# Kernel optimization log

Hardware: AMD Instinct MI355X
Metric: run time of the kernel (lower is better)

## Reference

```python
import jax, jax.numpy as jnp
import numpy as np

B, S, D, H = 2, 2048, 2048, 16
HD = D // H  # head_dim = 128

def _rope_tables(head_dim, context_length, theta_base=10000.0):
    inv_freq = 1.0 / theta_base ** (jnp.arange(0, head_dim, 2, dtype=jnp.float32) / head_dim)
    pos = jnp.arange(context_length, dtype=jnp.float32)
    angles = pos[:, None] * inv_freq[None, :]            # [S, HD/2]
    angles = jnp.concatenate([angles, angles], axis=1)   # [S, HD]
    return jnp.cos(angles), jnp.sin(angles)

def _apply_rope(x, cos, sin):
    # x: [b, h, s, hd]; cos/sin: [s, hd]
    hd = x.shape[-1]
    x1, x2 = x[..., : hd // 2], x[..., hd // 2 :]
    rotated = jnp.concatenate([-x2, x1], axis=-1)
    return x * cos[None, None] + rotated * sin[None, None]

def setup_inputs() -> dict:
    key = jax.random.key(0)
    ks = jax.random.split(key, 5)
    x = jax.random.normal(ks[0], (B, S, D), dtype=jnp.float32)
    scale = 1.0 / np.sqrt(D)
    Wq = jax.random.normal(ks[1], (D, D), dtype=jnp.float32) * scale
    Wk = jax.random.normal(ks[2], (D, D), dtype=jnp.float32) * scale
    Wv = jax.random.normal(ks[3], (D, D), dtype=jnp.float32) * scale
    Wo = jax.random.normal(ks[4], (D, D), dtype=jnp.float32) * scale
    cos, sin = _rope_tables(HD, S)
    return {"x": x, "Wq": Wq, "Wk": Wk, "Wv": Wv, "Wo": Wo, "cos": cos, "sin": sin}

def reference(x, Wq, Wk, Wv, Wo, cos, sin):
    b, s, _ = x.shape
    def split_heads(t):  # [b,s,D] -> [b,H,s,HD]
        return t.reshape(b, s, H, HD).transpose(0, 2, 1, 3)
    q = split_heads(x @ Wq.T)
    k = split_heads(x @ Wk.T)
    v = split_heads(x @ Wv.T)
    q = _apply_rope(q, cos[:s], sin[:s])
    k = _apply_rope(k, cos[:s], sin[:s])
    scores = jnp.einsum("bhqd,bhkd->bhqk", q, k) / np.sqrt(HD)
    causal = jnp.triu(jnp.ones((s, s), dtype=bool), k=1)
    scores = jnp.where(causal[None, None], -jnp.inf, scores)
    weights = jax.nn.softmax(scores, axis=-1)
    ctx = jnp.einsum("bhqk,bhkd->bhqd", weights, v)
    ctx = ctx.transpose(0, 2, 1, 3).reshape(b, s, D)
    return ctx @ Wo.T
```

## Files before the change

kernel.cpp:

```cpp
#include <hip/hip_runtime.h>
#include <cstdint>
#include <cmath>

#define B_ 2
#define S_ 2048
#define D_ 2048
#define H_ 16
#define HD_ 128

#define NEG_SENTINEL -1.0e30f

typedef __bf16 bf16;
typedef __attribute__((ext_vector_type(4))) __bf16 bf16x4;
typedef __attribute__((ext_vector_type(8))) __bf16 bf16x8;
typedef __attribute__((ext_vector_type(4))) float f32x4;

__device__ __forceinline__ void gload_lds16(const void* g, void* l) {
  __builtin_amdgcn_global_load_lds(
      (const __attribute__((address_space(1))) unsigned int*)g,
      (__attribute__((address_space(3))) unsigned int*)l, 16, 0, 0);
}

__device__ __forceinline__ f32x4 mfma16(bf16x8 a, bf16x8 b, f32x4 c) {
  return __builtin_amdgcn_mfma_f32_16x16x32_bf16(a, b, c, 0, 0, 0);
}

__global__ __launch_bounds__(256) void cvt_f32_bf16(
    const float* __restrict__ in, bf16* __restrict__ out)
{
  int i = blockIdx.x * 256 + threadIdx.x;
  f32x4 v = ((const f32x4*)in)[i];
  bf16x4 o;
#pragma unroll
  for (int j = 0; j < 4; ++j) o[j] = (bf16)v[j];
  ((bf16x4*)out)[i] = o;
}

#define GTM 128
#define GTN 128
#define GBK 64

template <typename OT>
__global__ __launch_bounds__(256) void gemm_xwt(
    const bf16* __restrict__ A, const bf16* __restrict__ W, OT* __restrict__ C,
    int M, int N, int K, int ldc)
{
  __shared__ bf16 sA[GTM * GBK];
  __shared__ bf16 sB[GTN * GBK];
  const int tid  = threadIdx.x;
  const int wave = tid >> 6, lane = tid & 63;
  const int quad = lane >> 4, l16 = lane & 15;
  const int tm = blockIdx.y * GTM;
  const int tn = blockIdx.x * GTN;
  const int wm = (wave >> 1) * 64, wn = (wave & 1) * 64;

  f32x4 acc[4][4];
#pragma unroll
  for (int i = 0; i < 4; ++i)
#pragma unroll
    for (int j = 0; j < 4; ++j) acc[i][j] = (f32x4)0.0f;

  for (int k0 = 0; k0 < K; k0 += GBK) {
    __syncthreads();
#pragma unroll
    for (int g = 0; g < 4; ++g) {
      int gb  = (g * 4 + wave) * 64;
      int p   = gb + lane;
      int row = p >> 3, pos = p & 7;
      int cc  = pos ^ (row & 7);
      gload_lds16(A + (size_t)(tm + row) * K + k0 + cc * 8, (char*)sA + (size_t)gb * 16);
      gload_lds16(W + (size_t)(tn + row) * K + k0 + cc * 8, (char*)sB + (size_t)gb * 16);
    }
    __syncthreads();

#pragma unroll
    for (int t = 0; t < 2; ++t) {
      bf16x8 af[4], bfr[4];
#pragma unroll
      for (int i = 0; i < 4; ++i) {
        int rowa = wm + i * 16 + l16;
        int posa = (t * 4 + quad) ^ (rowa & 7);
        af[i] = *(const bf16x8*)(sA + rowa * GBK + posa * 8);
        int rowb = wn + i * 16 + l16;
        int posb = (t * 4 + quad) ^ (rowb & 7);
        bfr[i] = *(const bf16x8*)(sB + rowb * GBK + posb * 8);
      }
#pragma unroll
      for (int i = 0; i < 4; ++i)
#pragma unroll
        for (int j = 0; j < 4; ++j)
          acc[i][j] = mfma16(af[i], bfr[j], acc[i][j]);
    }
  }

#pragma unroll
  for (int i = 0; i < 4; ++i)
#pragma unroll
    for (int r = 0; r < 4; ++r) {
      int row = tm + wm + i * 16 + quad * 4 + r;
#pragma unroll
      for (int j = 0; j < 4; ++j) {
        int col = tn + wn + j * 16 + l16;
        C[(size_t)row * ldc + col] = (OT)acc[i][j][r];
      }
    }
}

__global__ __launch_bounds__(256) void rope_qk(
    bf16* __restrict__ Q, bf16* __restrict__ Kk,
    const float* __restrict__ cosT, const float* __restrict__ sinT, int rs)
{
  const float kappa = 0.08838834764831845f * 1.4426950408889634f;
  int t = blockIdx.x * 256 + threadIdx.x;
  int d = t & 63;
  int h = (t >> 6) & (H_ - 1);
  int s = (t >> 10) & (S_ - 1);
  int b = t >> 21;
  size_t base = ((size_t)(b * S_ + s)) * rs + (size_t)h * HD_;
  float c1 = cosT[s * HD_ + d];
  float s1 = sinT[s * HD_ + d];
  float c2 = cosT[s * HD_ + d + 64];
  float s2 = sinT[s * HD_ + d + 64];
  {
    float x1 = (float)Q[base + d], x2 = (float)Q[base + d + 64];
    Q[base + d]      = (bf16)((x1 * c1 - x2 * s1) * kappa);
    Q[base + d + 64] = (bf16)((x2 * c2 + x1 * s2) * kappa);
  }
  {
    float x1 = (float)Kk[base + d], x2 = (float)Kk[base + d + 64];
    Kk[base + d]      = (bf16)(x1 * c1 - x2 * s1);
    Kk[base + d + 64] = (bf16)(x2 * c2 + x1 * s2);
  }
}

__global__ __launch_bounds__(256) void transpose_v(
    const bf16* __restrict__ V, bf16* __restrict__ Vt, int rs)
{
  __shared__ bf16 sT[64 * 72];
  const int tid = threadIdx.x;
  const int si = blockIdx.x;
  const int di = blockIdx.y;
  const int bh = blockIdx.z;
  const int b  = bh >> 4, h = bh & 15;

  const bf16* src = V + (size_t)b * S_ * rs + (size_t)h * HD_ + di * 64;
  bf16*       dst = Vt + ((size_t)bh * HD_ + di * 64) * S_ + si * 64;

#pragma unroll
  for (int half = 0; half < 2; ++half) {
    int r  = half * 32 + (tid >> 3);
    int c0 = (tid & 7) * 8;
    bf16x8 v = *(const bf16x8*)(src + (size_t)(si * 64 + r) * rs + c0);
    *(bf16x8*)(sT + r * 72 + c0) = v;
  }
  __syncthreads();
#pragma unroll
  for (int half = 0; half < 2; ++half) {
    int dr = half * 32 + (tid >> 3);
    int c0 = (tid & 7) * 8;
    bf16x8 o;
#pragma unroll
    for (int j = 0; j < 8; ++j) o[j] = sT[(c0 + j) * 72 + dr];
    *(bf16x8*)(dst + (size_t)dr * S_ + c0) = o;
  }
}

#define ABK 64
#define SPS 72

__global__ __launch_bounds__(256) void attn_fwd(
    const bf16* __restrict__ Q, const bf16* __restrict__ K,
    const bf16* __restrict__ Vt, bf16* __restrict__ O, int rs)
{
  __shared__ bf16 sK[ABK * HD_];
  __shared__ bf16 sVT[HD_ * ABK];
  __shared__ bf16 sP[64 * SPS];

  const int tid  = threadIdx.x;
  const int wave = tid >> 6, lane = tid & 63;
  const int quad = lane >> 4, l16 = lane & 15;

  const int lin   = (int)blockIdx.x;
  const int low3  = lin & 7;
  const int rest  = lin >> 3;
  const int pairx = rest & 15;
  const int colhi = rest >> 4;
  const int col   = low3 + (colhi << 3);
  const int b = col >> 4, h = col & 15;

  const bf16* Qh  = Q + (size_t)b * S_ * rs + (size_t)h * HD_;
  const bf16* Kh  = K + (size_t)b * S_ * rs + (size_t)h * HD_;
  const bf16* Vth = Vt + ((size_t)(b * H_ + h) * HD_) * S_;
  bf16*       Oh  = O + (size_t)b * S_ * D_ + (size_t)h * HD_;

  const int wq = wave * 16;

#pragma unroll 1
  for (int seg = 0; seg < 2; ++seg) {
    const int qt = seg == 0 ? pairx : 31 - pairx;
    const int q0 = qt * 64;
    const int wq_abs = q0 + wq;

    bf16x8 qf[4];
    {
      const bf16* rp = Qh + (size_t)(wq_abs + l16) * rs + quad * 8;
#pragma unroll
      for (int t = 0; t < 4; ++t) qf[t] = *(const bf16x8*)(rp + t * 32);
    }

    f32x4 o_acc[8];
#pragma unroll
    for (int j = 0; j < 8; ++j) o_acc[j] = (f32x4)0.0f;
    float m_col = NEG_SENTINEL;
    float l_col = 0.0f;

    const int nkt = qt + 1;
#pragma unroll 1
    for (int kt = 0; kt < nkt; ++kt) {
      const int kk0 = kt * ABK;
      __syncthreads();

#pragma unroll
      for (int g = 0; g < 4; ++g) {
        int p   = g * 256 + tid;
        int row = p >> 4, pos = p & 15;
        int cc  = pos ^ (row & 15);
        gload_lds16(Kh + (size_t)(kk0 + row) * rs + cc * 8, (char*)sK + (size_t)p * 16);
      }
#pragma unroll
      for (int g = 0; g < 4; ++g) {
        int p  = g * 256 + tid;
        int d  = p >> 3, pos = p & 7;
        int cc = pos ^ (d & 7);
        gload_lds16(Vth + (size_t)d * S_ + kk0 + cc * 8, (char*)sVT + (size_t)p * 16);
      }
      __syncthreads();

      if (kk0 <= wq_abs + 15) {
        f32x4 st[4];
#pragma unroll
        for (int jt = 0; jt < 4; ++jt) {
          bf16x8 kf[4];
#pragma unroll
          for (int t = 0; t < 4; ++t) {
            int pos = (t * 4 + quad) ^ l16;
            kf[t] = *(const bf16x8*)(sK + (jt * 16 + l16) * HD_ + pos * 8);
          }
          f32x4 a = (f32x4)0.0f;
#pragma unroll
          for (int t = 0; t < 4; ++t) a = mfma16(kf[t], qf[t], a);
          st[jt] = a;
        }

        if (kk0 + 63 > wq_abs) {
          int qcol = wq_abs + l16;
#pragma unroll
          for (int jt = 0; jt < 4; ++jt)
#pragma unroll
            for (int r = 0; r < 4; ++r) {
              int key = kk0 + jt * 16 + quad * 4 + r;
              if (key > qcol) st[jt][r] = NEG_SENTINEL;
            }
        }

        float mx = NEG_SENTINEL;
#pragma unroll
        for (int jt = 0; jt < 4; ++jt)
#pragma unroll
          for (int r = 0; r < 4; ++r) mx = fmaxf(mx, st[jt][r]);
        mx = fmaxf(mx, __shfl_xor(mx, 16, 64));
        mx = fmaxf(mx, __shfl_xor(mx, 32, 64));
        float m_new = fmaxf(m_col, mx);
        float alpha = exp2f(m_col - m_new);
        float ts = 0.0f;
#pragma unroll
        for (int jt = 0; jt < 4; ++jt) {
          bf16x4 pk;
#pragma unroll
          for (int r = 0; r < 4; ++r) {
            float p = exp2f(st[jt][r] - m_new);
            ts += p;
            pk[r] = (bf16)p;
          }
          *(bf16x4*)(sP + (wq + l16) * SPS + jt * 16 + quad * 4) = pk;
        }
        ts += __shfl_xor(ts, 16, 64);
        ts += __shfl_xor(ts, 32, 64);
        l_col = l_col * alpha + ts;
        m_col = m_new;
#pragma unroll
        for (int r = 0; r < 4; ++r) {
          float av = __shfl(alpha, quad * 4 + r, 64);
#pragma unroll
          for (int jd = 0; jd < 8; ++jd) o_acc[jd][r] *= av;
        }

#pragma unroll
        for (int ks = 0; ks < 2; ++ks) {
          bf16x8 pf = *(const bf16x8*)(sP + (wq + l16) * SPS + ks * 32 + quad * 8);
#pragma unroll
          for (int jd = 0; jd < 8; ++jd) {
            int pos = (ks * 4 + quad) ^ (l16 & 7);
            bf16x8 vf = *(const bf16x8*)(sVT + (jd * 16 + l16) * ABK + pos * 8);
            o_acc[jd] = mfma16(pf, vf, o_acc[jd]);
          }
        }
      }
    }

#pragma unroll
    for (int r = 0; r < 4; ++r) {
      float lv = __shfl(l_col, quad * 4 + r, 64);
      float inv_l = 1.0f / lv;
      int row = wq_abs + quad * 4 + r;
#pragma unroll
      for (int jd = 0; jd < 8; ++jd) {
        int colo = jd * 16 + l16;
        Oh[(size_t)row * D_ + colo] = (bf16)(o_acc[jd][r] * inv_l);
      }
    }
  }
}

extern "C" void kernel_launch(void* const* d_in, const int* in_sizes, int n_in,
                              void* d_out, int out_size, void* d_ws, size_t ws_size,
                              hipStream_t stream) {
  const float* x    = (const float*)d_in[0];
  const float* Wq   = (const float*)d_in[1];
  const float* Wk   = (const float*)d_in[2];
  const float* Wv   = (const float*)d_in[3];
  const float* Wo   = (const float*)d_in[4];
  const float* cosT = (const float*)d_in[5];
  const float* sinT = (const float*)d_in[6];
  float* out = (float*)d_out;

  const size_t NE = (size_t)B_ * S_ * D_;
  const size_t WE = (size_t)D_ * D_;
  const int M = B_ * S_;
  const int cvtX = (int)(NE / 1024);
  const int cvtW = (int)(WE / 1024);

  if (ws_size >= (size_t)92274688) {
    bf16* QKV   = (bf16*)d_ws;
    bf16* xb    = QKV + (size_t)M * 6144;
    bf16* Wqkv  = xb + NE;
    bf16* ctx   = Wqkv;
    bf16* Wob   = Wqkv + 2 * WE;
    bf16* Vt    = xb;

    cvt_f32_bf16<<<cvtX, 256, 0, stream>>>(x, xb);
    cvt_f32_bf16<<<cvtW, 256, 0, stream>>>(Wq, Wqkv);
    cvt_f32_bf16<<<cvtW, 256, 0, stream>>>(Wk, Wqkv + WE);
    cvt_f32_bf16<<<cvtW, 256, 0, stream>>>(Wv, Wqkv + 2 * WE);
    gemm_xwt<bf16><<<dim3(48, 32), 256, 0, stream>>>(xb, Wqkv, QKV, M, 3 * D_, D_, 3 * D_);
    rope_qk<<<(B_ * S_ * H_ * 64) / 256, 256, 0, stream>>>(QKV, QKV + D_, cosT, sinT, 3 * D_);
    transpose_v<<<dim3(32, 2, 32), 256, 0, stream>>>(QKV + 2 * D_, Vt, 3 * D_);
    attn_fwd<<<512, 256, 0, stream>>>(QKV, QKV + D_, Vt, ctx, 3 * D_);
    cvt_f32_bf16<<<cvtW, 256, 0, stream>>>(Wo, Wob);
    gemm_xwt<float><<<dim3(16, 32), 256, 0, stream>>>(ctx, Wob, out, M, D_, D_, D_);
  } else {
    bf16* Qb    = (bf16*)d_ws;
    bf16* Kb    = Qb + NE;
    bf16* Vb    = Kb + NE;
    bf16* Cb    = Vb + NE;
    bf16* Wslot = Cb + NE;

    cvt_f32_bf16<<<cvtX, 256, 0, stream>>>(x, Cb);
    cvt_f32_bf16<<<cvtW, 256, 0, stream>>>(Wq, Wslot);
    gemm_xwt<bf16><<<dim3(16, 32), 256, 0, stream>>>(Cb, Wslot, Qb, M, D_, D_, D_);
    cvt_f32_bf16<<<cvtW, 256, 0, stream>>>(Wk, Wslot);
    gemm_xwt<bf16><<<dim3(16, 32), 256, 0, stream>>>(Cb, Wslot, Kb, M, D_, D_, D_);
    cvt_f32_bf16<<<cvtW, 256, 0, stream>>>(Wv, Wslot);
    gemm_xwt<bf16><<<dim3(16, 32), 256, 0, stream>>>(Cb, Wslot, Vb, M, D_, D_, D_);
    rope_qk<<<(B_ * S_ * H_ * 64) / 256, 256, 0, stream>>>(Qb, Kb, cosT, sinT, D_);
    transpose_v<<<dim3(32, 2, 32), 256, 0, stream>>>(Vb, Cb, D_);
    attn_fwd<<<512, 256, 0, stream>>>(Qb, Kb, Cb, Vb, D_);
    cvt_f32_bf16<<<cvtW, 256, 0, stream>>>(Wo, Wslot);
    gemm_xwt<float><<<dim3(16, 32), 256, 0, stream>>>(Vb, Wslot, out, M, D_, D_, D_);
  }
}
```

Before: 402.8 us.

## Replace projection GEMMs with double-buffered 256x128 pipelined GEMM kernel

Adds a new gemm_pipe kernel with 512 threads, 256x128 tiles, double-buffered LDS staging through direct global-to-LDS loads, split half-tile prefetch, and s_setprio around the MFMA bursts. It uses an XCD-aware block remap to improve L2 locality. The fused QKV projection and the output projection switch to it on the large-workspace path. The aim is to overlap global loads with MFMA work and raise arithmetic intensity, at the cost of 96KB of dynamic LDS, which limits occupancy and makes the hand-tuned vmcnt waits fragile.

```diff
diff --git a/kernel.cpp b/kernel.cpp
--- a/kernel.cpp
+++ b/kernel.cpp
@@ -23,6 +23,12 @@
 
 __device__ __forceinline__ f32x4 mfma16(bf16x8 a, bf16x8 b, f32x4 c) {
   return __builtin_amdgcn_mfma_f32_16x16x32_bf16(a, b, c, 0, 0, 0);
+}
+
+__device__ __forceinline__ void wg_barrier() {
+  asm volatile("" ::: "memory");
+  __builtin_amdgcn_s_barrier();
+  asm volatile("" ::: "memory");
 }
 
 __global__ __launch_bounds__(256) void cvt_f32_bf16(
@@ -100,6 +106,138 @@
       int row = tm + wm + i * 16 + quad * 4 + r;
 #pragma unroll
       for (int j = 0; j < 4; ++j) {
+        int col = tn + wn + j * 16 + l16;
+        C[(size_t)row * ldc + col] = (OT)acc[i][j][r];
+      }
+    }
+}
+
+#define PTM 256
+#define PTN 128
+#define PBK 64
+#define PBUFB 49152
+#define PLDSB 98304
+
+#define STAGE_AU(kt_, u_) do { \
+    char* dstA_ = smem + (((kt_) & 1) * PBUFB); \
+    _Pragma("unroll") \
+    for (int g2_ = 0; g2_ < 2; ++g2_) { \
+      int row0_ = (u_) * 64 + g2_ * 128 + wave * 8; \
+      int row_  = row0_ + (lane >> 3); \
+      int cc_   = (lane & 7) ^ (row_ & 7); \
+      gload_lds16(A + (size_t)(tm + row_) * K + (size_t)(kt_) * PBK + cc_ * 8, \
+                  dstA_ + row0_ * 128); \
+    } } while (0)
+
+#define STAGE_BF(kt_) do { \
+    char* dstB_ = smem + (((kt_) & 1) * PBUFB) + 32768; \
+    _Pragma("unroll") \
+    for (int g2_ = 0; g2_ < 2; ++g2_) { \
+      int row0_ = g2_ * 64 + wave * 8; \
+      int row_  = row0_ + (lane >> 3); \
+      int cc_   = (lane & 7) ^ (row_ & 7); \
+      gload_lds16(W + (size_t)(tn + row_) * K + (size_t)(kt_) * PBK + cc_ * 8, \
+                  dstB_ + row0_ * 128); \
+    } } while (0)
+
+template <typename OT>
+__global__ __launch_bounds__(512, 2) void gemm_pipe(
+    const bf16* __restrict__ A, const bf16* __restrict__ W, OT* __restrict__ C,
+    int M, int N, int K, int ldc, int nby)
+{
+  extern __shared__ char smem[];
+  const int tid  = threadIdx.x;
+  const int wave = tid >> 6, lane = tid & 63;
+  const int quad = lane >> 4, l16 = lane & 15;
+
+  const int nwg = (int)gridDim.x;
+  const int cpx = nwg >> 3;
+  const int wg  = ((int)blockIdx.x & 7) * cpx + ((int)blockIdx.x >> 3);
+  const int bx = wg / nby, by = wg % nby;
+  const int tm = by * PTM, tn = bx * PTN;
+  const int wm = (wave >> 2) * 128, wn = (wave & 3) * 32;
+
+  const int NT = K / PBK;
+
+  f32x4 acc[8][2];
+#pragma unroll
+  for (int i = 0; i < 8; ++i)
+#pragma unroll
+    for (int j = 0; j < 2; ++j) acc[i][j] = (f32x4)0.0f;
+
+  STAGE_AU(0, 0);
+  STAGE_AU(0, 1);
+  STAGE_BF(0);
+  if (NT > 1) STAGE_AU(1, 0);
+  asm volatile("s_waitcnt vmcnt(2)" ::: "memory");
+  wg_barrier();
+
+#pragma unroll 1
+  for (int t = 0; t < NT; ++t) {
+    const bf16* sAb = (const bf16*)(smem + (t & 1) * PBUFB);
+    const bf16* sBb = sAb + 16384;
+    bf16x8 a[4][2], b[2][2];
+
+#pragma unroll
+    for (int i = 0; i < 4; ++i)
+#pragma unroll
+      for (int t2 = 0; t2 < 2; ++t2) {
+        int r  = wm + i * 16 + l16;
+        int ps = (t2 * 4 + quad) ^ (r & 7);
+        a[i][t2] = *(const bf16x8*)(sAb + r * 64 + ps * 8);
+      }
+#pragma unroll
+    for (int j = 0; j < 2; ++j)
+#pragma unroll
+      for (int t2 = 0; t2 < 2; ++t2) {
+        int r  = wn + j * 16 + l16;
+        int ps = (t2 * 4 + quad) ^ (r & 7);
+        b[j][t2] = *(const bf16x8*)(sBb + r * 64 + ps * 8);
+      }
+    if (t + 1 < NT) { STAGE_AU(t + 1, 1); STAGE_BF(t + 1); }
+    wg_barrier();
+    __builtin_amdgcn_s_setprio(1);
+#pragma unroll
+    for (int i = 0; i < 4; ++i)
+#pragma unroll
+      for (int j = 0; j < 2; ++j)
+#pragma unroll
+        for (int t2 = 0; t2 < 2; ++t2)
+          acc[i][j] = mfma16(a[i][t2], b[j][t2], acc[i][j]);
+    __builtin_amdgcn_s_setprio(0);
+    wg_barrier();
+
+#pragma unroll
+    for (int i = 0; i < 4; ++i)
+#pragma unroll
+      for (int t2 = 0; t2 < 2; ++t2) {
+        int r  = wm + 64 + i * 16 + l16;
+        int ps = (t2 * 4 + quad) ^ (r & 7);
+        a[i][t2] = *(const bf16x8*)(sAb + r * 64 + ps * 8);
+      }
+    if (t + 2 < NT) STAGE_AU(t + 2, 0);
+    wg_barrier();
+    __builtin_amdgcn_s_setprio(1);
+#pragma unroll
+    for (int i = 0; i < 4; ++i)
+#pragma unroll
+      for (int j = 0; j < 2; ++j)
+#pragma unroll
+        for (int t2 = 0; t2 < 2; ++t2)
+          acc[4 + i][j] = mfma16(a[i][t2], b[j][t2], acc[4 + i][j]);
+    __builtin_amdgcn_s_setprio(0);
+    if (t + 2 >= NT) { asm volatile("s_waitcnt vmcnt(0)" ::: "memory"); }
+    else             { asm volatile("s_waitcnt vmcnt(2)" ::: "memory"); }
+    wg_barrier();
+  }
+
+#pragma unroll
+  for (int i = 0; i < 8; ++i)
+#pragma unroll
+    for (int r = 0; r < 4; ++r) {
+      int row = tm + wm + i * 16 + quad * 4 + r;
+#pragma unroll
+      for (int j = 0; j < 2; ++j) {
         int col = tn + wn + j * 16 + l16;
         C[(size_t)row * ldc + col] = (OT)acc[i][j][r];
       }
@@ -340,6 +478,15 @@
   const int cvtX = (int)(NE / 1024);
   const int cvtW = (int)(WE / 1024);
 
+  static bool attr_done = false;
+  if (!attr_done) {
+    (void)hipFuncSetAttribute(reinterpret_cast<const void*>(gemm_pipe<bf16>),
+                              hipFuncAttributeMaxDynamicSharedMemorySize, PLDSB);
+    (void)hipFuncSetAttribute(reinterpret_cast<const void*>(gemm_pipe<float>),
+                              hipFuncAttributeMaxDynamicSharedMemorySize, PLDSB);
+    attr_done = true;
+  }
+
   if (ws_size >= (size_t)92274688) {
     bf16* QKV   = (bf16*)d_ws;
     bf16* xb    = QKV + (size_t)M * 6144;
@@ -352,12 +499,12 @@
     cvt_f32_bf16<<<cvtW, 256, 0, stream>>>(Wq, Wqkv);
     cvt_f32_bf16<<<cvtW, 256, 0, stream>>>(Wk, Wqkv + WE);
     cvt_f32_bf16<<<cvtW, 256, 0, stream>>>(Wv, Wqkv + 2 * WE);
-    gemm_xwt<bf16><<<dim3(48, 32), 256, 0, stream>>>(xb, Wqkv, QKV, M, 3 * D_, D_, 3 * D_);
+    gemm_pipe<bf16><<<768, 512, PLDSB, stream>>>(xb, Wqkv, QKV, M, 3 * D_, D_, 3 * D_, 16);
     rope_qk<<<(B_ * S_ * H_ * 64) / 256, 256, 0, stream>>>(QKV, QKV + D_, cosT, sinT, 3 * D_);
     transpose_v<<<dim3(32, 2, 32), 256, 0, stream>>>(QKV + 2 * D_, Vt, 3 * D_);
     attn_fwd<<<512, 256, 0, stream>>>(QKV, QKV + D_, Vt, ctx, 3 * D_);
     cvt_f32_bf16<<<cvtW, 256, 0, stream>>>(Wo, Wob);
-    gemm_xwt<float><<<dim3(16, 32), 256, 0, stream>>>(ctx, Wob, out, M, D_, D_, D_);
+    gemm_pipe<float><<<256, 512, PLDSB, stream>>>(ctx, Wob, out, M, D_, D_, D_, 16);
   } else {
     bf16* Qb    = (bf16*)d_ws;
     bf16* Kb    = Qb + NE;
```

Result: no change. 410.3 us (+1.9%).

## Replace QKV projection GEMM with 256x256 eight-phase pipelined kernel

Applied to the files above, without the earlier changes.

Adds a new bf16 GEMM for the fused QKV projection. It uses 256x256 tiles with 512 threads, double-buffered LDS loaded directly from global memory, and an eight-phase schedule that interleaves staging, LDS reads and MFMA under explicit waitcnt and barrier control. It also remaps workgroup IDs so blocks are grouped across dies. The aim is to hide global load latency and raise MFMA utilisation compared with the 128x128 GEMM. In exchange it needs 128KB of dynamic LDS and fragile hand-tuned wait counts, and the output projection still uses the old GEMM.

```diff
diff --git a/kernel.cpp b/kernel.cpp
--- a/kernel.cpp
+++ b/kernel.cpp
@@ -23,6 +23,12 @@
 
 __device__ __forceinline__ f32x4 mfma16(bf16x8 a, bf16x8 b, f32x4 c) {
   return __builtin_amdgcn_mfma_f32_16x16x32_bf16(a, b, c, 0, 0, 0);
+}
+
+__device__ __forceinline__ void wg_barrier() {
+  asm volatile("" ::: "memory");
+  __builtin_amdgcn_s_barrier();
+  asm volatile("" ::: "memory");
 }
 
 __global__ __launch_bounds__(256) void cvt_f32_bf16(
@@ -102,6 +108,192 @@
       for (int j = 0; j < 4; ++j) {
         int col = tn + wn + j * 16 + l16;
         C[(size_t)row * ldc + col] = (OT)acc[i][j][r];
+      }
+    }
+}
+
+#define QTM 256
+#define QTN 256
+#define QBK 64
+#define QHALF 16384
+#define QBUF 65536
+#define QLDS 131072
+
+#define QSTAGE_A(kt_, h_, bi_) do { \
+    char* dst_ = smem + (bi_) * QBUF + (h_) * QHALF; \
+    _Pragma("unroll") \
+    for (int g_ = 0; g_ < 2; ++g_) { \
+      int p_   = g_ * 512 + tid; \
+      int row_ = p_ >> 3; \
+      int cc_  = (p_ & 7) ^ (row_ & 7); \
+      gload_lds16(A + (size_t)(tm + (h_) * 128 + row_) * K + (size_t)(kt_) * QBK + cc_ * 8, \
+                  dst_ + (size_t)p_ * 16); \
+    } } while (0)
+
+#define QSTAGE_B(kt_, h_, bi_) do { \
+    char* dst_ = smem + (bi_) * QBUF + 32768 + (h_) * QHALF; \
+    _Pragma("unroll") \
+    for (int g_ = 0; g_ < 2; ++g_) { \
+      int p_   = g_ * 512 + tid; \
+      int row_ = p_ >> 3; \
+      int cc_  = (p_ & 7) ^ (row_ & 7); \
+      gload_lds16(W + (size_t)(tn + (h_) * 128 + row_) * K + (size_t)(kt_) * QBK + cc_ * 8, \
+                  dst_ + (size_t)p_ * 16); \
+    } } while (0)
+
+#define QREAD_A(Ab_, rh_) \
+    _Pragma("unroll") \
+    for (int i_ = 0; i_ < 4; ++i_) \
+    _Pragma("unroll") \
+    for (int t2_ = 0; t2_ < 2; ++t2_) { \
+      int rr_ = (rh_) * 64 + i_ * 16 + l16; \
+      int ps_ = (t2_ * 4 + quad) ^ (rr_ & 7); \
+      a[i_][t2_] = *(const bf16x8*)((Ab_) + rr_ * 64 + ps_ * 8); \
+    }
+
+#define QREAD_B(Bb_, bv_, ch_) \
+    _Pragma("unroll") \
+    for (int j_ = 0; j_ < 2; ++j_) \
+    _Pragma("unroll") \
+    for (int t2_ = 0; t2_ < 2; ++t2_) { \
+      int rb_ = wn64 + (ch_) * 32 + j_ * 16 + l16; \
+      int ps_ = (t2_ * 4 + quad) ^ (rb_ & 7); \
+      bv_[j_][t2_] = *(const bf16x8*)((Bb_) + rb_ * 64 + ps_ * 8); \
+    }
+
+#define QMFMA(rh_, ch_, bv_) \
+    __builtin_amdgcn_s_setprio(1); \
+    _Pragma("unroll") \
+    for (int i_ = 0; i_ < 4; ++i_) \
+    _Pragma("unroll") \
+    for (int j_ = 0; j_ < 2; ++j_) \
+    _Pragma("unroll") \
+    for (int t2_ = 0; t2_ < 2; ++t2_) \
+      acc[(rh_) * 4 + i_][(ch_) * 2 + j_] = \
+          mfma16(a[i_][t2_], bv_[j_][t2_], acc[(rh_) * 4 + i_][(ch_) * 2 + j_]); \
+    __builtin_amdgcn_s_setprio(0);
+
+#define LGK0()  asm volatile("s_waitcnt lgkmcnt(0)" ::: "memory")
+#define LGK8()  asm volatile("s_waitcnt lgkmcnt(8)" ::: "memory")
+#define VM4()   asm volatile("s_waitcnt vmcnt(4)" ::: "memory")
+#define VM0()   asm volatile("s_waitcnt vmcnt(0)" ::: "memory")
+
+__global__ __launch_bounds__(512, 2) void gemm_8ph(
+    const bf16* __restrict__ A, const bf16* __restrict__ W, bf16* __restrict__ C,
+    int M, int N, int K, int ldc, int nby)
+{
+  extern __shared__ char smem[];
+  const int tid  = threadIdx.x;
+  const int wave = tid >> 6, lane = tid & 63;
+  const int quad = lane >> 4, l16 = lane & 15;
+
+  const int nwg = (int)gridDim.x;
+  const int cpx = nwg >> 3;
+  const int wg  = ((int)blockIdx.x & 7) * cpx + ((int)blockIdx.x >> 3);
+  const int bx = wg / nby, by = wg % nby;
+  const int tm = by * QTM, tn = bx * QTN;
+  const int wm = (wave >> 2) * 128;
+  const int wn = (wave & 3) * 64;
+  const int wn64 = wn & 64;
+
+  const bf16* A0 = (const bf16*)(smem + (wm >> 7) * QHALF);
+  const bf16* B0 = (const bf16*)(smem + 32768 + (wn >> 7) * QHALF);
+  const bf16* A1 = (const bf16*)(smem + QBUF + (wm >> 7) * QHALF);
+  const bf16* B1 = (const bf16*)(smem + QBUF + 32768 + (wn >> 7) * QHALF);
+
+  const int NT = K / QBK;
+  const int NI = NT >> 1;
+
+  f32x4 acc[8][4];
+#pragma unroll
+  for (int i = 0; i < 8; ++i)
+#pragma unroll
+    for (int j = 0; j < 4; ++j) acc[i][j] = (f32x4)0.0f;
+
+  bf16x8 a[4][2], b0[2][2], b1[2][2];
+
+  QSTAGE_A(0, 0, 0);
+  QSTAGE_A(0, 1, 0);
+  QSTAGE_B(0, 0, 0);
+  QSTAGE_B(0, 1, 0);
+  QSTAGE_B(1, 0, 1);
+  QSTAGE_B(1, 1, 1);
+  VM4();
+  wg_barrier();
+
+#pragma unroll 1
+  for (int it = 0; it < NI; ++it) {
+    const int t0 = it * 2, t1 = t0 + 1;
+    const bool last = (it == NI - 1);
+
+    QREAD_A(A0, 0);
+    QREAD_B(B0, b0, 0);
+    QSTAGE_A(t1, 0, 1);
+    LGK8();
+    wg_barrier();
+    LGK0();
+    QMFMA(0, 0, b0);
+    wg_barrier();
+
+    QREAD_B(B0, b1, 1);
+    QSTAGE_A(t1, 1, 1);
+    wg_barrier();
+    LGK0();
+    QMFMA(0, 1, b1);
+    wg_barrier();
+
+    QREAD_A(A0, 1);
+    if (!last) QSTAGE_B(t0 + 2, 0, 0);
+    wg_barrier();
+    LGK0();
+    QMFMA(1, 1, b1);
+    wg_barrier();
+
+    if (!last) QSTAGE_B(t0 + 2, 1, 0);
+    wg_barrier();
+    QMFMA(1, 0, b0);
+    if (last) { VM0(); } else { VM4(); }
+    wg_barrier();
+
+    QREAD_A(A1, 0);
+    QREAD_B(B1, b0, 0);
+    if (!last) QSTAGE_A(t0 + 2, 0, 0);
+    LGK8();
+    wg_barrier();
+    LGK0();
+    QMFMA(0, 0, b0);
+    wg_barrier();
+
+    QREAD_B(B1, b1, 1);
+    if (!last) QSTAGE_A(t0 + 2, 1, 0);
+    wg_barrier();
+    LGK0();
+    QMFMA(0, 1, b1);
+    wg_barrier();
+
+    QREAD_A(A1, 1);
+    if (!last) QSTAGE_B(t1 + 2, 0, 1);
+    wg_barrier();
+    LGK0();
+    QMFMA(1, 1, b1);
+    wg_barrier();
+
+    if (!last) QSTAGE_B(t1 + 2, 1, 1);
+    wg_barrier();
+    QMFMA(1, 0, b0);
+    if (!last) { VM4(); }
+    wg_barrier();
+  }
+
+#pragma unroll
+  for (int ii = 0; ii < 8; ++ii)
+#pragma unroll
+    for (int r = 0; r < 4; ++r) {
+      int row = tm + wm + (ii >> 2) * 64 + (ii & 3) * 16 + quad * 4 + r;
+#pragma unroll
+      for (int jj = 0; jj < 4; ++jj) {
+        int col = tn + wn + jj * 16 + l16;
+        C[(size_t)row * ldc + col] = (bf16)acc[ii][jj][r];
       }
     }
 }
@@ -246,10 +438,10 @@
             int pos = (t * 4 + quad) ^ l16;
             kf[t] = *(const bf16x8*)(sK + (jt * 16 + l16) * HD_ + pos * 8);
           }
-          f32x4 a = (f32x4)0.0f;
-#pragma unroll
-          for (int t = 0; t < 4; ++t) a = mfma16(kf[t], qf[t], a);
-          st[jt] = a;
+          f32x4 a2 = (f32x4)0.0f;
+#pragma unroll
+          for (int t = 0; t < 4; ++t) a2 = mfma16(kf[t], qf[t], a2);
+          st[jt] = a2;
         }
 
         if (kk0 + 63 > wq_abs) {
@@ -340,6 +532,13 @@
   const int cvtX = (int)(NE / 1024);
   const int cvtW = (int)(WE / 1024);
 
+  static bool attr_done = false;
+  if (!attr_done) {
+    (void)hipFuncSetAttribute(reinterpret_cast<const void*>(gemm_8ph),
+                              hipFuncAttributeMaxDynamicSharedMemorySize, QLDS);
+    attr_done = true;
+  }
+
   if (ws_size >= (size_t)92274688) {
     bf16* QKV   = (bf16*)d_ws;
     bf16* xb    = QKV + (size_t)M * 6144;
@@ -352,7 +551,7 @@
     cvt_f32_bf16<<<cvtW, 256, 0, stream>>>(Wq, Wqkv);
     cvt_f32_bf16<<<cvtW, 256, 0, stream>>>(Wk, Wqkv + WE);
     cvt_f32_bf16<<<cvtW, 256, 0, stream>>>(Wv, Wqkv + 2 * WE);
-    gemm_xwt<bf16><<<dim3(48, 32), 256, 0, stream>>>(xb, Wqkv, QKV, M, 3 * D_, D_, 3 * D_);
+    gemm_8ph<<<384, 512, QLDS, stream>>>(xb, Wqkv, QKV, M, 3 * D_, D_, 3 * D_, 16);
     rope_qk<<<(B_ * S_ * H_ * 64) / 256, 256, 0, stream>>>(QKV, QKV + D_, cosT, sinT, 3 * D_);
     transpose_v<<<dim3(32, 2, 32), 256, 0, stream>>>(QKV + 2 * D_, Vt, 3 * D_);
     attn_fwd<<<512, 256, 0, stream>>>(QKV, QKV + D_, Vt, ctx, 3 * D_);
```

Measured after the change: 399.6 us. No clear change (-0.8%).

## Double-buffer K/V tiles in attention kernel with async prefetch

Applied to the files above, without the earlier changes.

Moves attention K and V^T staging into dynamic shared memory with two buffers. The next tile's global-to-LDS loads are issued before computing on the current tile, so load latency overlaps with the MFMA work. One waitcnt and barrier per iteration replace the two syncthreads around each load. The cost is roughly 73KB of LDS per block, which may lower occupancy to one or two blocks per CU.

```diff
diff --git a/kernel.cpp b/kernel.cpp
--- a/kernel.cpp
+++ b/kernel.cpp
@@ -24,6 +24,14 @@
 __device__ __forceinline__ f32x4 mfma16(bf16x8 a, bf16x8 b, f32x4 c) {
   return __builtin_amdgcn_mfma_f32_16x16x32_bf16(a, b, c, 0, 0, 0);
 }
+
+__device__ __forceinline__ void wg_barrier() {
+  asm volatile("" ::: "memory");
+  __builtin_amdgcn_s_barrier();
+  asm volatile("" ::: "memory");
+}
+
+#define AVM0() asm volatile("s_waitcnt vmcnt(0)" ::: "memory")
 
 __global__ __launch_bounds__(256) void cvt_f32_bf16(
     const float* __restrict__ in, bf16* __restrict__ out)
@@ -167,14 +175,36 @@
 
 #define ABK 64
 #define SPS 72
+#define ALDS 74752
+
+#define AK_STAGE(kt_, b_) do { \
+    int kk_ = (kt_) * ABK; \
+    _Pragma("unroll") \
+    for (int g_ = 0; g_ < 4; ++g_) { \
+      int p_   = g_ * 256 + tid; \
+      int row_ = p_ >> 4, pos_ = p_ & 15; \
+      int cc_  = pos_ ^ (row_ & 15); \
+      gload_lds16(Kh + (size_t)(kk_ + row_) * rs + cc_ * 8, \
+                  smem + (b_) * 16384 + (size_t)p_ * 16); \
+    } } while (0)
+
+#define AV_STAGE(kt_, b_) do { \
+    int kk_ = (kt_) * ABK; \
+    _Pragma("unroll") \
+    for (int g_ = 0; g_ < 4; ++g_) { \
+      int p_  = g_ * 256 + tid; \
+      int d_  = p_ >> 3, pos_ = p_ & 7; \
+      int cc_ = pos_ ^ (d_ & 7); \
+      gload_lds16(Vth + (size_t)d_ * S_ + kk_ + cc_ * 8, \
+                  smem + 32768 + (b_) * 16384 + (size_t)p_ * 16); \
+    } } while (0)
 
 __global__ __launch_bounds__(256) void attn_fwd(
     const bf16* __restrict__ Q, const bf16* __restrict__ K,
     const bf16* __restrict__ Vt, bf16* __restrict__ O, int rs)
 {
-  __shared__ bf16 sK[ABK * HD_];
-  __shared__ bf16 sVT[HD_ * ABK];
-  __shared__ bf16 sP[64 * SPS];
+  extern __shared__ char smem[];
+  bf16* sP = (bf16*)(smem + 65536);
 
   const int tid  = threadIdx.x;
   const int wave = tid >> 6, lane = tid & 63;
@@ -215,26 +245,23 @@
     float l_col = 0.0f;
 
     const int nkt = qt + 1;
+
+    AK_STAGE(0, 0);
+    AV_STAGE(0, 0);
+    AVM0();
+    wg_barrier();
+
+    int cur = 0;
 #pragma unroll 1
     for (int kt = 0; kt < nkt; ++kt) {
       const int kk0 = kt * ABK;
-      __syncthreads();
-
-#pragma unroll
-      for (int g = 0; g < 4; ++g) {
-        int p   = g * 256 + tid;
-        int row = p >> 4, pos = p & 15;
-        int cc  = pos ^ (row & 15);
-        gload_lds16(Kh + (size_t)(kk0 + row) * rs + cc * 8, (char*)sK + (size_t)p * 16);
+      const bf16* sKc = (const bf16*)(smem + cur * 16384);
+      const bf16* sVc = (const bf16*)(smem + 32768 + cur * 16384);
+
+      if (kt + 1 < nkt) {
+        AK_STAGE(kt + 1, cur ^ 1);
+        AV_STAGE(kt + 1, cur ^ 1);
       }
-#pragma unroll
-      for (int g = 0; g < 4; ++g) {
-        int p  = g * 256 + tid;
-        int d  = p >> 3, pos = p & 7;
-        int cc = pos ^ (d & 7);
-        gload_lds16(Vth + (size_t)d * S_ + kk0 + cc * 8, (char*)sVT + (size_t)p * 16);
-      }
-      __syncthreads();
 
       if (kk0 <= wq_abs + 15) {
         f32x4 st[4];
@@ -244,12 +271,12 @@
 #pragma unroll
           for (int t = 0; t < 4; ++t) {
             int pos = (t * 4 + quad) ^ l16;
-            kf[t] = *(const bf16x8*)(sK + (jt * 16 + l16) * HD_ + pos * 8);
+            kf[t] = *(const bf16x8*)(sKc + (jt * 16 + l16) * HD_ + pos * 8);
           }
-          f32x4 a = (f32x4)0.0f;
-#pragma unroll
-          for (int t = 0; t < 4; ++t) a = mfma16(kf[t], qf[t], a);
-          st[jt] = a;
+          f32x4 a2 = (f32x4)0.0f;
+#pragma unroll
+          for (int t = 0; t < 4; ++t) a2 = mfma16(kf[t], qf[t], a2);
+          st[jt] = a2;
         }
 
         if (kk0 + 63 > wq_abs) {
@@ -301,11 +328,15 @@
 #pragma unroll
           for (int jd = 0; jd < 8; ++jd) {
             int pos = (ks * 4 + quad) ^ (l16 & 7);
-            bf16x8 vf = *(const bf16x8*)(sVT + (jd * 16 + l16) * ABK + pos * 8);
+            bf16x8 vf = *(const bf16x8*)(sVc + (jd * 16 + l16) * ABK + pos * 8);
             o_acc[jd] = mfma16(pf, vf, o_acc[jd]);
           }
         }
       }
+
+      AVM0();
+      wg_barrier();
+      cur ^= 1;
     }
 
 #pragma unroll
@@ -340,6 +371,13 @@
   const int cvtX = (int)(NE / 1024);
   const int cvtW = (int)(WE / 1024);
 
+  static bool attr_done = false;
+  if (!attr_done) {
+    (void)hipFuncSetAttribute(reinterpret_cast<const void*>(attn_fwd),
+                              hipFuncAttributeMaxDynamicSharedMemorySize, ALDS);
+    attr_done = true;
+  }
+
   if (ws_size >= (size_t)92274688) {
     bf16* QKV   = (bf16*)d_ws;
     bf16* xb    = QKV + (size_t)M * 6144;
@@ -355,7 +393,7 @@
     gemm_xwt<bf16><<<dim3(48, 32), 256, 0, stream>>>(xb, Wqkv, QKV, M, 3 * D_, D_, 3 * D_);
     rope_qk<<<(B_ * S_ * H_ * 64) / 256, 256, 0, stream>>>(QKV, QKV + D_, cosT, sinT, 3 * D_);
     transpose_v<<<dim3(32, 2, 32), 256, 0, stream>>>(QKV + 2 * D_, Vt, 3 * D_);
-    attn_fwd<<<512, 256, 0, stream>>>(QKV, QKV + D_, Vt, ctx, 3 * D_);
+    attn_fwd<<<512, 256, ALDS, stream>>>(QKV, QKV + D_, Vt, ctx, 3 * D_);
     cvt_f32_bf16<<<cvtW, 256, 0, stream>>>(Wo, Wob);
     gemm_xwt<float><<<dim3(16, 32), 256, 0, stream>>>(ctx, Wob, out, M, D_, D_, D_);
   } else {
@@ -374,7 +412,7 @@
     gemm_xwt<bf16><<<dim3(16, 32), 256, 0, stream>>>(Cb, Wslot, Vb, M, D_, D_, D_);
     rope_qk<<<(B_ * S_ * H_ * 64) / 256, 256, 0, stream>>>(Qb, Kb, cosT, sinT, D_);
     transpose_v<<<dim3(32, 2, 32), 256, 0, stream>>>(Vb, Cb, D_);
-    attn_fwd<<<512, 256, 0, stream>>>(Qb, Kb, Cb, Vb, D_);
+    attn_fwd<<<512, 256, ALDS, stream>>>(Qb, Kb, Cb, Vb, D_);
     cvt_f32_bf16<<<cvtW, 256, 0, stream>>>(Wo, Wslot);
     gemm_xwt<float><<<dim3(16, 32), 256, 0, stream>>>(Vb, Wslot, out, M, D_, D_, D_);
   }
```

New measurement: 409.2 us. Within noise of the previous version (+1.6%).
